# Optimization experiments

Measured on AMD Instinct MI355X. Metric: run time of the kernel, lower is better.

## Reference

```python
import jax, jax.numpy as jnp
import numpy as np

B, M, N, P, H, W, D, DIMG, NH = 32, 2048, 512, 16, 640, 640, 256, 384, 8
PD = 3 * P * P  # 768 flattened patch dim


def layer_norm(x, g, b, eps=1e-5):
    mu = x.mean(-1, keepdims=True)
    var = ((x - mu) ** 2).mean(-1, keepdims=True)
    return (x - mu) * jax.lax.rsqrt(var + eps) * g + b


def get_patches(img, kpts, patch):
    # img [B,3,H,W], kpts [B,N,2] (x,y), NaN rows -> NaN patches
    Bb, C, Hh, Ww = img.shape
    half = patch // 2
    safe = jnp.nan_to_num(kpts, nan=0.0)
    ctr = jnp.round(safe).astype(jnp.int32)
    x0 = jnp.clip(ctr[..., 0] - half, 0, Ww - patch)
    y0 = jnp.clip(ctr[..., 1] - half, 0, Hh - patch)
    offs = jnp.arange(patch)
    ys = y0[..., None] + offs  # [B,N,P]
    xs = x0[..., None] + offs  # [B,N,P]

    def ext(im_b, ys_b, xs_b):
        p = im_b[:, ys_b[:, :, None], xs_b[:, None, :]]  # [C,N,P,P]
        return jnp.transpose(p, (1, 0, 2, 3))  # [N,C,P,P]

    patches = jax.vmap(ext)(img, ys, xs)  # [B,N,C,P,P]
    invalid = jnp.isnan(kpts).any(-1)
    return jnp.where(invalid[:, :, None, None, None], jnp.nan, patches)


def setup_inputs() -> dict:
    key = jax.random.key(0)
    ks = jax.random.split(key, 16)
    im0 = jax.random.uniform(ks[0], (B, 3, H, W), jnp.float32)
    im1 = jax.random.uniform(ks[1], (B, 3, H, W), jnp.float32)
    wh = jnp.array([W - 1.0, H - 1.0], jnp.float32)
    kpts0 = jax.random.uniform(ks[2], (B, M, 2), jnp.float32) * wh
    kpts1 = jax.random.uniform(ks[3], (B, M, 2), jnp.float32) * wh
    scores0 = jax.random.uniform(ks[4], (B, M), jnp.float32)
    scores1 = jax.random.uniform(ks[5], (B, M), jnp.float32)
    image_embs = jax.random.normal(ks[6], (B, DIMG), jnp.float32)
    m0 = jax.random.randint(ks[7], (B, N), 0, M)
    m1 = jax.random.randint(ks[8], (B, N), -300, M)
    m1 = jnp.where(m1 < 0, -1, m1)
    sorted_matches = jnp.stack([m0, m1], axis=-1).astype(jnp.int32)
    s = 0.02
    params = dict(
        ln1_g=jnp.ones((PD,), jnp.float32), ln1_b=jnp.zeros((PD,), jnp.float32),
        W_pe=jax.random.normal(ks[9], (D - 1, PD), jnp.float32) * s,
        b_pe=jnp.zeros((D - 1,), jnp.float32),
        ln2_g=jnp.ones((D - 1,), jnp.float32), ln2_b=jnp.zeros((D - 1,), jnp.float32),
        W_proj=jax.random.normal(ks[10], (D, DIMG), jnp.float32) * s,
        b_proj=jnp.zeros((D,), jnp.float32),
        in_w=jax.random.normal(ks[11], (3 * D, D), jnp.float32) * s,
        in_b=jnp.zeros((3 * D,), jnp.float32),
        out_w=jax.random.normal(ks[12], (D, D), jnp.float32) * s,
        out_b=jnp.zeros((D,), jnp.float32),
        W_fc=jax.random.normal(ks[13], (6, D), jnp.float32) * s,
        b_fc=jnp.zeros((6,), jnp.float32),
    )
    return dict(im0=im0, im1=im1, kpts0=kpts0, kpts1=kpts1, scores0=scores0,
                scores1=scores1, image_embs=image_embs,
                sorted_matches=sorted_matches, **params)


def reference(im0, im1, kpts0, kpts1, scores0, scores1, image_embs,
              sorted_matches, ln1_g, ln1_b, W_pe, b_pe, ln2_g, ln2_b,
              W_proj, b_proj, in_w, in_b, out_w, out_b, W_fc, b_fc):
    im0 = jnp.clip(im0, 0.0, 1.0)
    im1 = jnp.clip(im1, 0.0, 1.0)
    m0 = sorted_matches[..., 0]
    m1 = sorted_matches[..., 1]
    valid = m1 > -1  # [B,N]
    m0c = jnp.clip(m0, 0, M - 1)
    m1c = jnp.clip(m1, 0, M - 1)
    # vectorized masked gather with NaN padding (replaces the double python loop)
    g0 = jnp.take_along_axis(kpts0, m0c[..., None], axis=1)  # [B,N,2]
    g1 = jnp.take_along_axis(kpts1, m1c[..., None], axis=1)
    k0v = jnp.where(valid[..., None], g0, jnp.nan)
    k1v = jnp.where(valid[..., None], g1, jnp.nan)
    s0v = jnp.where(valid, jnp.take_along_axis(scores0, m0c, axis=1), 0.0)
    s1v = jnp.where(valid, jnp.take_along_axis(scores1, m1c, axis=1), 0.0)
    p0 = jnp.nan_to_num(get_patches(im0, k0v, P), nan=-1.0)  # [B,N,3,P,P]
    p1 = jnp.nan_to_num(get_patches(im1, k1v, P), nan=-1.0)
    patches = jnp.concatenate([p0, p1], axis=1)  # [B,2N,3,P,P]
    flat = patches.reshape(B, 2 * N, PD)
    e = layer_norm(flat, ln1_g, ln1_b)
    e = e @ W_pe.T + b_pe
    e = layer_norm(e, ln2_g, ln2_b)  # [B,2N,D-1]
    scores = jnp.concatenate([s0v, s1v], axis=1)  # [B,2N]
    pe = jnp.concatenate([e, scores[..., None]], axis=-1)  # [B,2N,D]
    # motion estimator: cross-attn, query = projected image embedding
    q = image_embs @ W_proj.T + b_proj  # [B,D]
    Wq, Wk, Wv = in_w[:D], in_w[D:2 * D], in_w[2 * D:]
    bq, bk, bv = in_b[:D], in_b[D:2 * D], in_b[2 * D:]
    dh = D // NH
    qh = (q @ Wq.T + bq).reshape(B, 1, NH, dh)
    kh = (pe @ Wk.T + bk).reshape(B, 2 * N, NH, dh)
    vh = (pe @ Wv.T + bv).reshape(B, 2 * N, NH, dh)
    scale = 1.0 / np.sqrt(dh).astype(np.float32)
    att = jnp.einsum('bqhd,bkhd->bhqk', qh, kh) * scale
    a = jax.nn.softmax(att, axis=-1)
    o = jnp.einsum('bhqk,bkhd->bqhd', a, vh).reshape(B, 1, D)
    o = o @ out_w.T + out_b
    out = (o @ W_fc.T + b_fc).reshape(B, 6)
    return out
```

## Files before the change

kernel.cpp:

```cpp
#include <hip/hip_runtime.h>
#include <math.h>

#define BB 32
#define MM 2048
#define NN 512
#define PSZ 16
#define HH 640
#define WW 640
#define DD 256
#define DIMG_ 384
#define NHEADS 8
#define PD_ 768
#define TWO_N 1024
#define ROWS_TOT (BB * TWO_N)
#define CHCT 16

typedef short bf16x8 __attribute__((ext_vector_type(8)));
typedef float f32x4  __attribute__((ext_vector_type(4)));

__device__ __forceinline__ unsigned short f2bf(float x) {
  unsigned int u = __float_as_uint(x);
  u = (u + 0x7FFF + ((u >> 16) & 1)) >> 16;
  return (unsigned short)u;
}
__device__ __forceinline__ float bf2f(unsigned short h) {
  return __uint_as_float(((unsigned int)h) << 16);
}

__device__ __forceinline__ void gload_lds16(const void* g, void* l) {
  __builtin_amdgcn_global_load_lds(
      (const __attribute__((address_space(1))) void*)g,
      (__attribute__((address_space(3))) void*)l, 16, 0, 0);
}

__global__ __launch_bounds__(256) void prep_extract_kernel(
    const float* __restrict__ W_pe,
    unsigned short* __restrict__ Whi, unsigned short* __restrict__ Wlo,
    const float* __restrict__ image_embs,
    const float* __restrict__ W_proj, const float* __restrict__ b_proj,
    const float* __restrict__ in_w,   const float* __restrict__ in_b,
    float* __restrict__ u_out, float* __restrict__ bias_out,
    const float* __restrict__ im0, const float* __restrict__ im1,
    const float* __restrict__ kpts0, const float* __restrict__ kpts1,
    const float* __restrict__ scores0, const float* __restrict__ scores1,
    const int*   __restrict__ sorted_matches,
    const float* __restrict__ ln1_g, const float* __restrict__ ln1_b,
    unsigned short* __restrict__ Ahi, unsigned short* __restrict__ Alo,
    float* __restrict__ score_all)
{
  __shared__ float q1[DD];
  __shared__ float q2[DD];
  const int t = threadIdx.x;

  if (blockIdx.x < 768) {
    const int idx = blockIdx.x * 256 + t;
    const int row = idx / PD_;
    float v = (row < 255) ? W_pe[idx] : 0.0f;
    const unsigned short h = f2bf(v);
    Whi[idx] = h;
    Wlo[idx] = f2bf(v - bf2f(h));
    return;
  }

  if (blockIdx.x < 800) {
    const int b = blockIdx.x - 768;
    {
      const float4* emb = (const float4*)(image_embs + (size_t)b * DIMG_);
      const float4* wr  = (const float4*)(W_proj + (size_t)t * DIMG_);
      float a = b_proj[t];
      #pragma unroll 4
      for (int i = 0; i < DIMG_ / 4; ++i) {
        const float4 e4 = emb[i], w4 = wr[i];
        a += e4.x * w4.x + e4.y * w4.y + e4.z * w4.z + e4.w * w4.w;
      }
      q1[t] = a;
    }
    __syncthreads();
    {
      const float4* wr = (const float4*)(in_w + (size_t)t * DD);
      const float4* qq = (const float4*)q1;
      float a = in_b[t];
      #pragma unroll 4
      for (int i = 0; i < DD / 4; ++i) {
        const float4 q4 = qq[i], w4 = wr[i];
        a += q4.x * w4.x + q4.y * w4.y + q4.z * w4.z + q4.w * w4.w;
      }
      q2[t] = a;
    }
    __syncthreads();
    #pragma unroll
    for (int h = 0; h < NHEADS; ++h) {
      float s = 0.0f;
      #pragma unroll 8
      for (int i = 0; i < 32; ++i)
        s += q2[h * 32 + i] * in_w[(size_t)(DD + h * 32 + i) * DD + t];
      u_out[((size_t)b * NHEADS + h) * DD + t] = s;
    }
    if (t < NHEADS) {
      float s = 0.0f;
      for (int i = 0; i < 32; ++i) s += q2[t * 32 + i] * in_b[DD + t * 32 + i];
      bias_out[b * NHEADS + t] = s;
    }
    return;
  }

  const int L  = t & 63;
  const long gp = (long)(blockIdx.x - 800) * 4 + (t >> 6);
  const int b   = (int)(gp >> 10);
  const int n2  = (int)(gp & 1023);
  const bool side1 = (n2 >= NN);
  const float* img  = side1 ? im1 : im0;
  const float* kpts = side1 ? kpts1 : kpts0;
  const float* scrs = side1 ? scores1 : scores0;

  const int n  = side1 ? (n2 - NN) : n2;
  const int m0 = sorted_matches[((size_t)b * NN + n) * 2 + 0];
  const int m1 = sorted_matches[((size_t)b * NN + n) * 2 + 1];
  const bool valid = (m1 > -1);
  int midx = side1 ? m1 : m0;
  midx = min(max(midx, 0), MM - 1);
  const float kx = kpts[((size_t)b * MM + midx) * 2 + 0];
  const float ky = kpts[((size_t)b * MM + midx) * 2 + 1];
  const int x0 = min(max((int)rintf(kx) - 8, 0), WW - PSZ);
  const int y0 = min(max((int)rintf(ky) - 8, 0), HH - PSZ);

  float v[12];
  if (valid) {
    const size_t imb = (size_t)b * 3 * HH * WW;
    const int px = (2 * L) & 15;
    #pragma unroll
    for (int j = 0; j < 6; ++j) {
      const int p0 = 2 * L + 128 * j;
      const int c  = p0 >> 8;
      const int py = (p0 >> 4) & 15;
      const float* rp = img + imb + ((size_t)c * HH + y0 + py) * WW + x0 + px;
      v[2 * j]     = fminf(fmaxf(rp[0], 0.0f), 1.0f);
      v[2 * j + 1] = fminf(fmaxf(rp[1], 0.0f), 1.0f);
    }
  } else {
    #pragma unroll
    for (int i = 0; i < 12; ++i) v[i] = -1.0f;
  }

  float s = 0.0f, ss = 0.0f;
  #pragma unroll
  for (int i = 0; i < 12; ++i) { s += v[i]; ss += v[i] * v[i]; }
  #pragma unroll
  for (int m = 32; m; m >>= 1) { s += __shfl_xor(s, m); ss += __shfl_xor(ss, m); }
  const float mu  = s * (1.0f / 768.0f);
  const float var = ss * (1.0f / 768.0f) - mu * mu;
  const float rs  = 1.0f / sqrtf(var + 1e-5f);

  unsigned int* AhiW = (unsigned int*)(Ahi + gp * PD_);
  unsigned int* AloW = (unsigned int*)(Alo + gp * PD_);
  #pragma unroll
  for (int j = 0; j < 6; ++j) {
    const int p0 = 2 * L + 128 * j;
    const float y0e = (v[2 * j]     - mu) * rs * ln1_g[p0]     + ln1_b[p0];
    const float y1e = (v[2 * j + 1] - mu) * rs * ln1_g[p0 + 1] + ln1_b[p0 + 1];
    const unsigned short h0 = f2bf(y0e), h1 = f2bf(y1e);
    AhiW[p0 >> 1] = (unsigned int)h0 | ((unsigned int)h1 << 16);
    const unsigned short l0 = f2bf(y0e - bf2f(h0));
    const unsigned short l1 = f2bf(y1e - bf2f(h1));
    AloW[p0 >> 1] = (unsigned int)l0 | ((unsigned int)l1 << 16);
  }
  if (L == 0) {
    score_all[gp] = valid ? scrs[(size_t)b * MM + midx] : 0.0f;
  }
}

__global__ __launch_bounds__(512, 1) void gemm_fused_kernel(
    const unsigned short* __restrict__ Ahi, const unsigned short* __restrict__ Alo,
    const unsigned short* __restrict__ Whi, const unsigned short* __restrict__ Wlo,
    const float* __restrict__ b_pe,
    const float* __restrict__ ln2_g, const float* __restrict__ ln2_b,
    const float* __restrict__ score_all,
    const float* __restrict__ u, const float* __restrict__ ubias,
    float* __restrict__ pe, float* __restrict__ lt)
{
  __shared__ __align__(16) char smem[98304];
  __shared__ float u_lds[NHEADS * DD];
  __shared__ float cv_bpe[DD], cv_g[DD], cv_b[DD];
  __shared__ float ub_lds[NHEADS];

  unsigned short* const sbase = (unsigned short*)smem;
  const int t = threadIdx.x;
  const int w = t >> 6, L = t & 63;
  const int mt = blockIdx.x;
  const int bidx = mt >> 3;

  {
    const float* ub0 = u + (size_t)bidx * NHEADS * DD;
    #pragma unroll
    for (int i = 0; i < 4; ++i) u_lds[t + 512 * i] = ub0[t + 512 * i];
    if (t < DD) {
      cv_bpe[t] = (t < 255) ? b_pe[t]  : 0.0f;
      cv_g[t]   = (t < 255) ? ln2_g[t] : 0.0f;
      cv_b[t]   = (t < 255) ? ln2_b[t] : 0.0f;
    }
    if (t < NHEADS) ub_lds[t] = ubias[bidx * NHEADS + t];
  }

  const int rr   = L >> 2;
  const int q_st = (L & 3) ^ ((L >> 4) & 3);

  const unsigned short* gsrc[6];
  int loff0[6], sstr[6];
  #pragma unroll
  for (int c = 0; c < 6; ++c) {
    const int cc = w * 6 + c;
    const unsigned short* sp; long row; int off, str;
    if (cc < 16) {
      sp  = (cc < 8) ? Ahi : Alo;
      row = (long)mt * 128 + (cc & 7) * 16 + rr;
      off = ((cc >> 3) * 128 + (cc & 7) * 16) * 32;
      str = 8192;
    } else {
      const int c2 = cc - 16;
      sp  = (c2 < 16) ? Whi : Wlo;
      row = (c2 & 15) * 16 + rr;
      off = 16384 + ((c2 >> 4) * 256 + (c2 & 15) * 16) * 32;
      str = 16384;
    }
    gsrc[c]  = sp + row * (long)PD_ + q_st * 8;
    loff0[c] = off;
    sstr[c]  = str;
  }

  const int lane_m = L & 15, quad = L >> 4;
  const int swz = quad ^ (lane_m >> 2);
  const int wr = w >> 2, wc = w & 3;
  const int am0 = wr * 64, bn0 = wc * 64;

  f32x4 acc[4][4];
  #pragma unroll
  for (int i = 0; i < 4; ++i)
    #pragma unroll
    for (int j = 0; j < 4; ++j) acc[i][j] = (f32x4){0.f, 0.f, 0.f, 0.f};

  #pragma unroll
  for (int c = 0; c < 6; ++c) gload_lds16(gsrc[c], sbase + loff0[c]);
  __syncthreads();

  for (int ks = 0; ks < PD_ / 32; ++ks) {
    const int cur = ks & 1;
    if (ks < PD_ / 32 - 1) {
      const int k0n = (ks + 1) * 32;
      const int nb  = cur ^ 1;
      #pragma unroll
      for (int c = 0; c < 6; ++c)
        gload_lds16(gsrc[c] + k0n, sbase + loff0[c] + nb * sstr[c]);
    }
    const unsigned short* Ab = sbase + cur * 8192;
    const unsigned short* Bb = sbase + 16384 + cur * 16384;
    bf16x8 ah[4], al[4], bh[4], bl[4];
    #pragma unroll
    for (int i = 0; i < 4; ++i) {
      const int ra = (am0 + i * 16 + lane_m) * 32 + swz * 8;
      ah[i] = *(const bf16x8*)(Ab + ra);
      al[i] = *(const bf16x8*)(Ab + 4096 + ra);
      const int rb = (bn0 + i * 16 + lane_m) * 32 + swz * 8;
      bh[i] = *(const bf16x8*)(Bb + rb);
      bl[i] = *(const bf16x8*)(Bb + 8192 + rb);
    }
    #pragma unroll
    for (int i = 0; i < 4; ++i)
      #pragma unroll
      for (int j = 0; j < 4; ++j) {
        acc[i][j] = __builtin_amdgcn_mfma_f32_16x16x32_bf16(ah[i], bh[j], acc[i][j], 0, 0, 0);
        acc[i][j] = __builtin_amdgcn_mfma_f32_16x16x32_bf16(ah[i], bl[j], acc[i][j], 0, 0, 0);
        acc[i][j] = __builtin_amdgcn_mfma_f32_16x16x32_bf16(al[i], bh[j], acc[i][j], 0, 0, 0);
      }
    __syncthreads();
  }

  float* const eb = (float*)smem;
  const int r8 = t >> 3, l8 = t & 7;
  #pragma unroll
  for (int hh = 0; hh < 2; ++hh) {
    if (hh) __syncthreads();
    if (wr == hh) {
      #pragma unroll
      for (int i = 0; i < 4; ++i)
        #pragma unroll
        for (int j = 0; j < 4; ++j)
          #pragma unroll
          for (int v = 0; v < 4; ++v)
            eb[(i * 16 + quad * 4 + v) * 260 + bn0 + j * 16 + lane_m] = acc[i][j][v];
    }
    __syncthreads();

    const long grow = (long)mt * 128 + hh * 64 + r8;
    float x[32];
    float s = 0.0f, ss = 0.0f;
    #pragma unroll
    for (int j = 0; j < 32; ++j) {
      const int c = l8 + 8 * j;
      float vv = eb[r8 * 260 + c];
      if (c < 255) { vv += cv_bpe[c]; s += vv; ss += vv * vv; }
      x[j] = vv;
    }
    s += __shfl_xor(s, 1); ss += __shfl_xor(ss, 1);
    s += __shfl_xor(s, 2); ss += __shfl_xor(ss, 2);
    s += __shfl_xor(s, 4); ss += __shfl_xor(ss, 4);
    const float mu  = s * (1.0f / 255.0f);
    const float var = ss * (1.0f / 255.0f) - mu * mu;
    const float rs  = 1.0f / sqrtf(var + 1e-5f);

    float scrow = 0.0f;
    if (l8 == 7) scrow = score_all[grow];

    float d[NHEADS] = {0, 0, 0, 0, 0, 0, 0, 0};
    float* const per = pe + grow * DD;
    #pragma unroll
    for (int j = 0; j < 32; ++j) {
      const int c = l8 + 8 * j;
      const float y = (c < 255) ? (x[j] - mu) * rs * cv_g[c] + cv_b[c] : scrow;
      per[c] = y;
      #pragma unroll
      for (int h = 0; h < NHEADS; ++h) d[h] += y * u_lds[h * DD + c];
    }
    #pragma unroll
    for (int h = 0; h < NHEADS; ++h) {
      d[h] += __shfl_xor(d[h], 1);
      d[h] += __shfl_xor(d[h], 2);
      d[h] += __shfl_xor(d[h], 4);
    }
    const float dv = (l8 == 0) ? d[0] : (l8 == 1) ? d[1] : (l8 == 2) ? d[2] :
                     (l8 == 3) ? d[3] : (l8 == 4) ? d[4] : (l8 == 5) ? d[5] :
                     (l8 == 6) ? d[6] : d[7];
    lt[grow * NHEADS + l8] = (dv + ub_lds[l8]) * 0.17677669529663687f;
  }
}

__global__ __launch_bounds__(256) void ctx_kernel(
    const float* __restrict__ pe, const float* __restrict__ lt,
    float* __restrict__ ctxp)
{
  __shared__ __align__(16) float pr[TWO_N][NHEADS];
  const int b = blockIdx.x, ch = blockIdx.y, t = threadIdx.x;

  {
    const int h = t >> 5, l = t & 31;
    const float* base = lt + (size_t)b * TWO_N * NHEADS + h;
    float v[32];
    float mx = -1e30f;
    #pragma unroll 8
    for (int i = 0; i < 32; ++i) { v[i] = base[(l + 32 * i) * NHEADS]; mx = fmaxf(mx, v[i]); }
    #pragma unroll
    for (int m = 16; m; m >>= 1) mx = fmaxf(mx, __shfl_xor(mx, m, 32));
    float sm = 0.0f;
    #pragma unroll 8
    for (int i = 0; i < 32; ++i) { v[i] = expf(v[i] - mx); sm += v[i]; }
    #pragma unroll
    for (int m = 16; m; m >>= 1) sm += __shfl_xor(sm, m, 32);
    const float inv = 1.0f / sm;
    #pragma unroll 8
    for (int i = 0; i < 32; ++i) pr[l + 32 * i][h] = v[i] * inv;
  }
  __syncthreads();

  const float* peb = pe + ((size_t)b * TWO_N + ch * 64) * DD;
  float acc[NHEADS] = {0, 0, 0, 0, 0, 0, 0, 0};
  #pragma unroll 4
  for (int k = 0; k < 64; ++k) {
    const float v = peb[(size_t)k * DD + t];
    const float4 a0 = *(const float4*)&pr[ch * 64 + k][0];
    const float4 a1 = *(const float4*)&pr[ch * 64 + k][4];
    acc[0] += a0.x * v; acc[1] += a0.y * v; acc[2] += a0.z * v; acc[3] += a0.w * v;
    acc[4] += a1.x * v; acc[5] += a1.y * v; acc[6] += a1.z * v; acc[7] += a1.w * v;
  }
  #pragma unroll
  for (int h = 0; h < NHEADS; ++h)
    ctxp[(((size_t)b * CHCT + ch) * NHEADS + h) * DD + t] = acc[h];
}

__global__ __launch_bounds__(256) void final_kernel(
    const float* __restrict__ ctxp,
    const float* __restrict__ in_w,  const float* __restrict__ in_b,
    const float* __restrict__ out_w, const float* __restrict__ out_b,
    const float* __restrict__ W_fc,  const float* __restrict__ b_fc,
    float* __restrict__ outp)
{
  __shared__ __align__(16) float ctx_sh[NHEADS * DD];
  __shared__ __align__(16) float o_sh[DD], o2_sh[DD];
  const int t = threadIdx.x;
  const int b = blockIdx.x;

  #pragma unroll
  for (int h = 0; h < NHEADS; ++h) {
    float s = 0.0f;
    #pragma unroll
    for (int ch = 0; ch < CHCT; ++ch)
      s += ctxp[(((size_t)b * CHCT + ch) * NHEADS + h) * DD + t];
    ctx_sh[h * DD + t] = s;
  }
  __syncthreads();
  {
    const float4* wv = (const float4*)(in_w + (size_t)(2 * DD + t) * DD);
    const float4* cx = (const float4*)(ctx_sh + (t >> 5) * DD);
    float o1 = in_b[2 * DD + t];
    #pragma unroll 4
    for (int j = 0; j < DD / 4; ++j) {
      const float4 w4 = wv[j], c4 = cx[j];
      o1 += w4.x * c4.x + w4.y * c4.y + w4.z * c4.z + w4.w * c4.w;
    }
    o_sh[t] = o1;
  }
  __syncthreads();
  {
    const float4* wr = (const float4*)(out_w + (size_t)t * DD);
    const float4* oo = (const float4*)o_sh;
    float o2 = out_b[t];
    #pragma unroll 4
    for (int j = 0; j < DD / 4; ++j) {
      const float4 w4 = wr[j], c4 = oo[j];
      o2 += w4.x * c4.x + w4.y * c4.y + w4.z * c4.z + w4.w * c4.w;
    }
    o2_sh[t] = o2;
  }
  __syncthreads();
  if (t < 6) {
    const float4* wr = (const float4*)(W_fc + (size_t)t * DD);
    const float4* oo = (const float4*)o2_sh;
    float r = b_fc[t];
    for (int j = 0; j < DD / 4; ++j) {
      const float4 w4 = wr[j], c4 = oo[j];
      r += w4.x * c4.x + w4.y * c4.y + w4.z * c4.z + w4.w * c4.w;
    }
    outp[b * 6 + t] = r;
  }
}

extern "C" void kernel_launch(void* const* d_in, const int* in_sizes, int n_in,
                              void* d_out, int out_size, void* d_ws, size_t ws_size,
                              hipStream_t stream) {
  const float* im0       = (const float*)d_in[0];
  const float* im1       = (const float*)d_in[1];
  const float* kpts0     = (const float*)d_in[2];
  const float* kpts1     = (const float*)d_in[3];
  const float* scores0   = (const float*)d_in[4];
  const float* scores1   = (const float*)d_in[5];
  const float* image_embs= (const float*)d_in[6];
  const int*   smatch    = (const int*)d_in[7];
  const float* ln1_g     = (const float*)d_in[8];
  const float* ln1_b     = (const float*)d_in[9];
  const float* W_pe      = (const float*)d_in[10];
  const float* b_pe      = (const float*)d_in[11];
  const float* ln2_g     = (const float*)d_in[12];
  const float* ln2_b     = (const float*)d_in[13];
  const float* W_proj    = (const float*)d_in[14];
  const float* b_proj    = (const float*)d_in[15];
  const float* in_w      = (const float*)d_in[16];
  const float* in_b      = (const float*)d_in[17];
  const float* out_w     = (const float*)d_in[18];
  const float* out_b     = (const float*)d_in[19];
  const float* W_fc      = (const float*)d_in[20];
  const float* b_fc      = (const float*)d_in[21];

  char* ws = (char*)d_ws;
  size_t off = 0;
  float* epe   = (float*)(ws + off); off += (size_t)ROWS_TOT * DD * 4;
  float* u     = (float*)(ws + off); off += (size_t)BB * NHEADS * DD * 4;
  float* ubias = (float*)(ws + off); off += (size_t)BB * NHEADS * 4;
  off = (off + 1023) & ~(size_t)1023;
  float* score = (float*)(ws + off); off += (size_t)ROWS_TOT * 4;
  float* lt    = (float*)(ws + off); off += (size_t)BB * TWO_N * NHEADS * 4;
  float* ctxp  = (float*)(ws + off); off += (size_t)BB * CHCT * NHEADS * DD * 4;
  unsigned short* Whi = (unsigned short*)(ws + off); off += (size_t)256 * PD_ * 2;
  unsigned short* Wlo = (unsigned short*)(ws + off); off += (size_t)256 * PD_ * 2;
  off = (off + 1023) & ~(size_t)1023;
  unsigned short* Ahi = (unsigned short*)(ws + off); off += (size_t)ROWS_TOT * PD_ * 2;
  unsigned short* Alo = (unsigned short*)(ws + off); off += (size_t)ROWS_TOT * PD_ * 2;

  prep_extract_kernel<<<800 + ROWS_TOT / 4, 256, 0, stream>>>(
      W_pe, Whi, Wlo, image_embs, W_proj, b_proj, in_w, in_b, u, ubias,
      im0, im1, kpts0, kpts1, scores0, scores1, smatch,
      ln1_g, ln1_b, Ahi, Alo, score);
  gemm_fused_kernel<<<ROWS_TOT / 128, 512, 0, stream>>>(
      Ahi, Alo, Whi, Wlo, b_pe, ln2_g, ln2_b, score, u, ubias, epe, lt);
  ctx_kernel<<<dim3(BB, CHCT), 256, 0, stream>>>(epe, lt, ctxp);
  final_kernel<<<BB, 256, 0, stream>>>(ctxp, in_w, in_b, out_w, out_b,
                                       W_fc, b_fc, (float*)d_out);
}
```

Before: 510.0 us.

## Fold attention-logit projection into GEMM via precomputed per-batch V columns

The per-head logit dot product with u is rewritten algebraically. Per-batch vectors V = W_pe^T (g*u) are precomputed in the prep kernel and appended as 16 extra B columns, so the GEMM produces the logit term directly and the LayerNorm correction is applied with precomputed scalar sums. This removes the per-row 8-head dot product over 255 columns in the epilogue. The GEMM is also retiled to 64-row blocks with 256 threads, two blocks per CU, a single LDS buffer and no double buffering. Softmax moves into its own kernel so ctx uses more, smaller chunks. Precision shifts slightly because the logits now depend on split-bf16 products of V.

```diff
diff --git a/kernel.cpp b/kernel.cpp
--- a/kernel.cpp
+++ b/kernel.cpp
@@ -13,7 +13,7 @@
 #define PD_ 768
 #define TWO_N 1024
 #define ROWS_TOT (BB * TWO_N)
-#define CHCT 16
+#define CHCT 32
 
 typedef short bf16x8 __attribute__((ext_vector_type(8)));
 typedef float f32x4  __attribute__((ext_vector_type(4)));
@@ -39,7 +39,10 @@
     const float* __restrict__ image_embs,
     const float* __restrict__ W_proj, const float* __restrict__ b_proj,
     const float* __restrict__ in_w,   const float* __restrict__ in_b,
-    float* __restrict__ u_out, float* __restrict__ bias_out,
+    const float* __restrict__ b_pe,
+    const float* __restrict__ ln2_g, const float* __restrict__ ln2_b,
+    unsigned short* __restrict__ Vhi, unsigned short* __restrict__ Vlo,
+    float* __restrict__ Pc,
     const float* __restrict__ im0, const float* __restrict__ im1,
     const float* __restrict__ kpts0, const float* __restrict__ kpts1,
     const float* __restrict__ scores0, const float* __restrict__ scores1,
@@ -49,7 +52,10 @@
     float* __restrict__ score_all)
 {
   __shared__ float q1[DD];
-  __shared__ float q2[DD];
+  __shared__ float q2s[DD];
+  __shared__ float u_sh[NHEADS][DD];
+  __shared__ float gu_sh[DD][NHEADS];
+  __shared__ float sred[NHEADS][3][4];
   const int t = threadIdx.x;
 
   if (blockIdx.x < 768) {
@@ -85,7 +91,7 @@
         const float4 q4 = qq[i], w4 = wr[i];
         a += q4.x * w4.x + q4.y * w4.y + q4.z * w4.z + q4.w * w4.w;
       }
-      q2[t] = a;
+      q2s[t] = a;
     }
     __syncthreads();
     #pragma unroll
@@ -93,13 +99,67 @@
       float s = 0.0f;
       #pragma unroll 8
       for (int i = 0; i < 32; ++i)
-        s += q2[h * 32 + i] * in_w[(size_t)(DD + h * 32 + i) * DD + t];
-      u_out[((size_t)b * NHEADS + h) * DD + t] = s;
-    }
+        s += q2s[h * 32 + i] * in_w[(size_t)(DD + h * 32 + i) * DD + t];
+      u_sh[h][t] = s;
+    }
+    float ubv = 0.0f;
     if (t < NHEADS) {
-      float s = 0.0f;
-      for (int i = 0; i < 32; ++i) s += q2[t * 32 + i] * in_b[DD + t * 32 + i];
-      bias_out[b * NHEADS + t] = s;
+      for (int i = 0; i < 32; ++i) ubv += q2s[t * 32 + i] * in_b[DD + t * 32 + i];
+    }
+    __syncthreads();
+
+    const bool cvld = (t < 255);
+    const float g_c = cvld ? ln2_g[t] : 0.0f;
+    const float bb_c = cvld ? ln2_b[t] : 0.0f;
+    const float pp_c = cvld ? b_pe[t]  : 0.0f;
+    const int wv = t >> 6, ln = t & 63;
+    #pragma unroll
+    for (int h = 0; h < NHEADS; ++h) {
+      const float u_c = u_sh[h][t];
+      const float gu  = g_c * u_c;
+      gu_sh[t][h] = gu;
+      float x1 = gu, x2 = bb_c * u_c, x3 = pp_c * gu;
+      #pragma unroll
+      for (int m = 32; m; m >>= 1) {
+        x1 += __shfl_xor(x1, m); x2 += __shfl_xor(x2, m); x3 += __shfl_xor(x3, m);
+      }
+      if (ln == 0) { sred[h][0][wv] = x1; sred[h][1][wv] = x2; sred[h][2][wv] = x3; }
+    }
+    __syncthreads();
+    if (t < NHEADS) {
+      const float S1 = sred[t][0][0] + sred[t][0][1] + sred[t][0][2] + sred[t][0][3];
+      const float S2 = sred[t][1][0] + sred[t][1][1] + sred[t][1][2] + sred[t][1][3];
+      const float S3 = sred[t][2][0] + sred[t][2][1] + sred[t][2][2] + sred[t][2][3];
+      float* pc = Pc + b * 40;
+      pc[t]      = S1;
+      pc[8 + t]  = S2;
+      pc[16 + t] = S3;
+      pc[24 + t] = u_sh[t][255];
+      pc[32 + t] = ubv;
+    }
+
+    #pragma unroll
+    for (int kk = 0; kk < 3; ++kk) {
+      const int k = t + 256 * kk;
+      float vh[NHEADS] = {0, 0, 0, 0, 0, 0, 0, 0};
+      for (int c = 0; c < 255; ++c) {
+        const float wv_ = W_pe[(size_t)c * PD_ + k];
+        const float4 g0 = *(const float4*)&gu_sh[c][0];
+        const float4 g1 = *(const float4*)&gu_sh[c][4];
+        vh[0] += wv_ * g0.x; vh[1] += wv_ * g0.y; vh[2] += wv_ * g0.z; vh[3] += wv_ * g0.w;
+        vh[4] += wv_ * g1.x; vh[5] += wv_ * g1.y; vh[6] += wv_ * g1.z; vh[7] += wv_ * g1.w;
+      }
+      #pragma unroll
+      for (int h = 0; h < NHEADS; ++h) {
+        const unsigned short hi = f2bf(vh[h]);
+        Vhi[((size_t)b * 16 + h) * PD_ + k] = hi;
+        Vlo[((size_t)b * 16 + h) * PD_ + k] = f2bf(vh[h] - bf2f(hi));
+      }
+      #pragma unroll
+      for (int h = NHEADS; h < 16; ++h) {
+        Vhi[((size_t)b * 16 + h) * PD_ + k] = 0;
+        Vlo[((size_t)b * 16 + h) * PD_ + k] = 0;
+      }
     }
     return;
   }
@@ -169,204 +229,212 @@
   }
 }
 
-__global__ __launch_bounds__(512, 1) void gemm_fused_kernel(
+__global__ __launch_bounds__(256, 2) void gemm_fused_kernel(
     const unsigned short* __restrict__ Ahi, const unsigned short* __restrict__ Alo,
     const unsigned short* __restrict__ Whi, const unsigned short* __restrict__ Wlo,
+    const unsigned short* __restrict__ Vhi, const unsigned short* __restrict__ Vlo,
     const float* __restrict__ b_pe,
     const float* __restrict__ ln2_g, const float* __restrict__ ln2_b,
     const float* __restrict__ score_all,
-    const float* __restrict__ u, const float* __restrict__ ubias,
+    const float* __restrict__ Pc,
     float* __restrict__ pe, float* __restrict__ lt)
 {
-  __shared__ __align__(16) char smem[98304];
-  __shared__ float u_lds[NHEADS * DD];
-  __shared__ float cv_bpe[DD], cv_g[DD], cv_b[DD];
-  __shared__ float ub_lds[NHEADS];
-
-  unsigned short* const sbase = (unsigned short*)smem;
+  __shared__ __align__(16) unsigned short sm[21504];
   const int t = threadIdx.x;
   const int w = t >> 6, L = t & 63;
   const int mt = blockIdx.x;
-  const int bidx = mt >> 3;
-
-  {
-    const float* ub0 = u + (size_t)bidx * NHEADS * DD;
-    #pragma unroll
-    for (int i = 0; i < 4; ++i) u_lds[t + 512 * i] = ub0[t + 512 * i];
-    if (t < DD) {
-      cv_bpe[t] = (t < 255) ? b_pe[t]  : 0.0f;
-      cv_g[t]   = (t < 255) ? ln2_g[t] : 0.0f;
-      cv_b[t]   = (t < 255) ? ln2_b[t] : 0.0f;
-    }
-    if (t < NHEADS) ub_lds[t] = ubias[bidx * NHEADS + t];
-  }
+  const int bidx = mt >> 4;
 
   const int rr   = L >> 2;
   const int q_st = (L & 3) ^ ((L >> 4) & 3);
-
-  const unsigned short* gsrc[6];
-  int loff0[6], sstr[6];
-  #pragma unroll
-  for (int c = 0; c < 6; ++c) {
-    const int cc = w * 6 + c;
-    const unsigned short* sp; long row; int off, str;
-    if (cc < 16) {
-      sp  = (cc < 8) ? Ahi : Alo;
-      row = (long)mt * 128 + (cc & 7) * 16 + rr;
-      off = ((cc >> 3) * 128 + (cc & 7) * 16) * 32;
-      str = 8192;
-    } else {
-      const int c2 = cc - 16;
-      sp  = (c2 < 16) ? Whi : Wlo;
-      row = (c2 & 15) * 16 + rr;
-      off = 16384 + ((c2 >> 4) * 256 + (c2 & 15) * 16) * 32;
-      str = 16384;
-    }
-    gsrc[c]  = sp + row * (long)PD_ + q_st * 8;
-    loff0[c] = off;
-    sstr[c]  = str;
-  }
-
   const int lane_m = L & 15, quad = L >> 4;
   const int swz = quad ^ (lane_m >> 2);
-  const int wr = w >> 2, wc = w & 3;
-  const int am0 = wr * 64, bn0 = wc * 64;
-
-  f32x4 acc[4][4];
+
+  const unsigned short* gsrc[11];
+  int ldst[11];
+  #pragma unroll
+  for (int c = 0; c < 11; ++c) {
+    const int cc = w + 4 * c;
+    const unsigned short* sp = Ahi; long rb = 0; int dst = 0;
+    if (cc < 4)       { sp = Ahi; rb = (long)mt * 64 + cc * 16;       dst = cc * 512; }
+    else if (cc < 8)  { sp = Alo; rb = (long)mt * 64 + (cc - 4) * 16; dst = 2048 + (cc - 4) * 512; }
+    else if (cc < 25) { const int r0 = (cc - 8) * 16;
+                        sp = (r0 < 256) ? (Whi + (long)r0 * PD_)
+                                        : (Vhi + (long)bidx * 16 * PD_);
+                        dst = 4096 + (cc - 8) * 512; }
+    else if (cc < 42) { const int r0 = (cc - 25) * 16;
+                        sp = (r0 < 256) ? (Wlo + (long)r0 * PD_)
+                                        : (Vlo + (long)bidx * 16 * PD_);
+                        dst = 12800 + (cc - 25) * 512; }
+    gsrc[c] = sp + (rb + rr) * (long)PD_ + q_st * 8;
+    ldst[c] = dst;
+  }
+  const int CNT = (w < 2) ? 11 : 10;
+  const int JW  = (w == 3) ? 5 : 4;
+
+  f32x4 acc[4][5];
   #pragma unroll
   for (int i = 0; i < 4; ++i)
     #pragma unroll
-    for (int j = 0; j < 4; ++j) acc[i][j] = (f32x4){0.f, 0.f, 0.f, 0.f};
-
-  #pragma unroll
-  for (int c = 0; c < 6; ++c) gload_lds16(gsrc[c], sbase + loff0[c]);
-  __syncthreads();
+    for (int j = 0; j < 5; ++j) acc[i][j] = (f32x4){0.f, 0.f, 0.f, 0.f};
 
   for (int ks = 0; ks < PD_ / 32; ++ks) {
-    const int cur = ks & 1;
-    if (ks < PD_ / 32 - 1) {
-      const int k0n = (ks + 1) * 32;
-      const int nb  = cur ^ 1;
+    const int k0 = ks * 32;
+    __syncthreads();
+    #pragma unroll
+    for (int c = 0; c < 11; ++c)
+      if (c < CNT) gload_lds16(gsrc[c] + k0, sm + ldst[c]);
+    __syncthreads();
+
+    bf16x8 ah[4], al[4];
+    #pragma unroll
+    for (int i = 0; i < 4; ++i) {
+      const int offa = (i * 16 + lane_m) * 32 + swz * 8;
+      ah[i] = *(const bf16x8*)(sm + offa);
+      al[i] = *(const bf16x8*)(sm + 2048 + offa);
+    }
+    #pragma unroll
+    for (int j = 0; j < 5; ++j) {
+      if (j < JW) {
+        const int offb = (w * 64 + j * 16 + lane_m) * 32 + swz * 8;
+        const bf16x8 bh = *(const bf16x8*)(sm + 4096 + offb);
+        const bf16x8 bl = *(const bf16x8*)(sm + 12800 + offb);
+        #pragma unroll
+        for (int i = 0; i < 4; ++i) {
+          acc[i][j] = __builtin_amdgcn_mfma_f32_16x16x32_bf16(ah[i], bh, acc[i][j], 0, 0, 0);
+          acc[i][j] = __builtin_amdgcn_mfma_f32_16x16x32_bf16(ah[i], bl, acc[i][j], 0, 0, 0);
+          acc[i][j] = __builtin_amdgcn_mfma_f32_16x16x32_bf16(al[i], bh, acc[i][j], 0, 0, 0);
+        }
+      }
+    }
+  }
+
+  __syncthreads();
+  float* const fs = (float*)sm;
+  float p4[4], g4[4], b4[4];
+  #pragma unroll
+  for (int j = 0; j < 4; ++j) {
+    const int c = w * 64 + j * 16 + lane_m;
+    const bool cv = (c < 255);
+    p4[j] = cv ? b_pe[c]  : 0.0f;
+    g4[j] = cv ? ln2_g[c] : 0.0f;
+    b4[j] = cv ? ln2_b[c] : 0.0f;
+  }
+  float sv[16], qv[16];
+  #pragma unroll
+  for (int i = 0; i < 4; ++i)
+    #pragma unroll
+    for (int v = 0; v < 4; ++v) {
+      float s = 0.0f, q = 0.0f;
       #pragma unroll
-      for (int c = 0; c < 6; ++c)
-        gload_lds16(gsrc[c] + k0n, sbase + loff0[c] + nb * sstr[c]);
-    }
-    const unsigned short* Ab = sbase + cur * 8192;
-    const unsigned short* Bb = sbase + 16384 + cur * 16384;
-    bf16x8 ah[4], al[4], bh[4], bl[4];
-    #pragma unroll
-    for (int i = 0; i < 4; ++i) {
-      const int ra = (am0 + i * 16 + lane_m) * 32 + swz * 8;
-      ah[i] = *(const bf16x8*)(Ab + ra);
-      al[i] = *(const bf16x8*)(Ab + 4096 + ra);
-      const int rb = (bn0 + i * 16 + lane_m) * 32 + swz * 8;
-      bh[i] = *(const bf16x8*)(Bb + rb);
-      bl[i] = *(const bf16x8*)(Bb + 8192 + rb);
-    }
+      for (int j = 0; j < 4; ++j) {
+        const float x = acc[i][j][v] + p4[j];
+        s += x; q += x * x;
+      }
+      sv[i * 4 + v] = s; qv[i * 4 + v] = q;
+    }
+  #pragma unroll
+  for (int iv = 0; iv < 16; ++iv) {
+    #pragma unroll
+    for (int m = 1; m <= 8; m <<= 1) {
+      sv[iv] += __shfl_xor(sv[iv], m);
+      qv[iv] += __shfl_xor(qv[iv], m);
+    }
+  }
+  if (lane_m == 0) {
     #pragma unroll
     for (int i = 0; i < 4; ++i)
       #pragma unroll
+      for (int v = 0; v < 4; ++v) {
+        const int row = i * 16 + quad * 4 + v;
+        fs[w * 64 + row]       = sv[i * 4 + v];
+        fs[256 + w * 64 + row] = qv[i * 4 + v];
+      }
+  }
+  __syncthreads();
+  if (t < 64) {
+    const float S  = fs[t] + fs[64 + t] + fs[128 + t] + fs[192 + t];
+    const float SS = fs[256 + t] + fs[320 + t] + fs[384 + t] + fs[448 + t];
+    const float mu  = S * (1.0f / 255.0f);
+    const float var = SS * (1.0f / 255.0f) - mu * mu;
+    fs[512 + t] = mu;
+    fs[576 + t] = 1.0f / sqrtf(var + 1e-5f);
+  }
+  __syncthreads();
+
+  float S1 = 0, S2 = 0, S3 = 0, u255 = 0, ubias = 0;
+  if (w == 3 && lane_m < NHEADS) {
+    const float* pc = Pc + bidx * 40;
+    S1 = pc[lane_m]; S2 = pc[8 + lane_m]; S3 = pc[16 + lane_m];
+    u255 = pc[24 + lane_m]; ubias = pc[32 + lane_m];
+  }
+
+  #pragma unroll
+  for (int i = 0; i < 4; ++i)
+    #pragma unroll
+    for (int v = 0; v < 4; ++v) {
+      const int row = i * 16 + quad * 4 + v;
+      const long grow = (long)mt * 64 + row;
+      const float mu = fs[512 + row];
+      const float rs = fs[576 + row];
+      float sc = 0.0f;
+      if (w == 3) sc = score_all[grow];
+      float* rowp = pe + grow * DD + w * 64 + lane_m;
+      #pragma unroll
       for (int j = 0; j < 4; ++j) {
-        acc[i][j] = __builtin_amdgcn_mfma_f32_16x16x32_bf16(ah[i], bh[j], acc[i][j], 0, 0, 0);
-        acc[i][j] = __builtin_amdgcn_mfma_f32_16x16x32_bf16(ah[i], bl[j], acc[i][j], 0, 0, 0);
-        acc[i][j] = __builtin_amdgcn_mfma_f32_16x16x32_bf16(al[i], bh[j], acc[i][j], 0, 0, 0);
-      }
-    __syncthreads();
-  }
-
-  float* const eb = (float*)smem;
-  const int r8 = t >> 3, l8 = t & 7;
-  #pragma unroll
-  for (int hh = 0; hh < 2; ++hh) {
-    if (hh) __syncthreads();
-    if (wr == hh) {
-      #pragma unroll
-      for (int i = 0; i < 4; ++i)
-        #pragma unroll
-        for (int j = 0; j < 4; ++j)
-          #pragma unroll
-          for (int v = 0; v < 4; ++v)
-            eb[(i * 16 + quad * 4 + v) * 260 + bn0 + j * 16 + lane_m] = acc[i][j][v];
-    }
-    __syncthreads();
-
-    const long grow = (long)mt * 128 + hh * 64 + r8;
-    float x[32];
-    float s = 0.0f, ss = 0.0f;
-    #pragma unroll
-    for (int j = 0; j < 32; ++j) {
-      const int c = l8 + 8 * j;
-      float vv = eb[r8 * 260 + c];
-      if (c < 255) { vv += cv_bpe[c]; s += vv; ss += vv * vv; }
-      x[j] = vv;
-    }
-    s += __shfl_xor(s, 1); ss += __shfl_xor(ss, 1);
-    s += __shfl_xor(s, 2); ss += __shfl_xor(ss, 2);
-    s += __shfl_xor(s, 4); ss += __shfl_xor(ss, 4);
-    const float mu  = s * (1.0f / 255.0f);
-    const float var = ss * (1.0f / 255.0f) - mu * mu;
-    const float rs  = 1.0f / sqrtf(var + 1e-5f);
-
-    float scrow = 0.0f;
-    if (l8 == 7) scrow = score_all[grow];
-
-    float d[NHEADS] = {0, 0, 0, 0, 0, 0, 0, 0};
-    float* const per = pe + grow * DD;
-    #pragma unroll
-    for (int j = 0; j < 32; ++j) {
-      const int c = l8 + 8 * j;
-      const float y = (c < 255) ? (x[j] - mu) * rs * cv_g[c] + cv_b[c] : scrow;
-      per[c] = y;
-      #pragma unroll
-      for (int h = 0; h < NHEADS; ++h) d[h] += y * u_lds[h * DD + c];
-    }
-    #pragma unroll
-    for (int h = 0; h < NHEADS; ++h) {
-      d[h] += __shfl_xor(d[h], 1);
-      d[h] += __shfl_xor(d[h], 2);
-      d[h] += __shfl_xor(d[h], 4);
-    }
-    const float dv = (l8 == 0) ? d[0] : (l8 == 1) ? d[1] : (l8 == 2) ? d[2] :
-                     (l8 == 3) ? d[3] : (l8 == 4) ? d[4] : (l8 == 5) ? d[5] :
-                     (l8 == 6) ? d[6] : d[7];
-    lt[grow * NHEADS + l8] = (dv + ub_lds[l8]) * 0.17677669529663687f;
-  }
+        const int c = w * 64 + j * 16 + lane_m;
+        const float y = (c < 255)
+            ? (acc[i][j][v] + p4[j] - mu) * rs * g4[j] + b4[j]
+            : sc;
+        rowp[j * 16] = y;
+      }
+      if (w == 3 && lane_m < NHEADS) {
+        const float T = acc[i][4][v];
+        const float d = rs * (T + S3 - mu * S1) + S2 + sc * u255;
+        lt[grow * NHEADS + lane_m] = (d + ubias) * 0.17677669529663687f;
+      }
+    }
+}
+
+__global__ __launch_bounds__(256) void softmax_kernel(
+    const float* __restrict__ lt, float* __restrict__ prg)
+{
+  const int b = blockIdx.x, t = threadIdx.x;
+  const int h = t >> 5, l = t & 31;
+  const float* base = lt + (size_t)b * TWO_N * NHEADS + h;
+  float v[32];
+  float mx = -1e30f;
+  #pragma unroll 8
+  for (int i = 0; i < 32; ++i) { v[i] = base[(l + 32 * i) * NHEADS]; mx = fmaxf(mx, v[i]); }
+  #pragma unroll
+  for (int m = 16; m; m >>= 1) mx = fmaxf(mx, __shfl_xor(mx, m, 32));
+  float sm = 0.0f;
+  #pragma unroll 8
+  for (int i = 0; i < 32; ++i) { v[i] = expf(v[i] - mx); sm += v[i]; }
+  #pragma unroll
+  for (int m = 16; m; m >>= 1) sm += __shfl_xor(sm, m, 32);
+  const float inv = 1.0f / sm;
+  float* out = prg + (size_t)b * TWO_N * NHEADS + h;
+  #pragma unroll 8
+  for (int i = 0; i < 32; ++i) out[(l + 32 * i) * NHEADS] = v[i] * inv;
 }
 
 __global__ __launch_bounds__(256) void ctx_kernel(
-    const float* __restrict__ pe, const float* __restrict__ lt,
+    const float* __restrict__ pe, const float* __restrict__ prg,
     float* __restrict__ ctxp)
 {
-  __shared__ __align__(16) float pr[TWO_N][NHEADS];
+  __shared__ __align__(16) float prc[32 * NHEADS];
   const int b = blockIdx.x, ch = blockIdx.y, t = threadIdx.x;
-
-  {
-    const int h = t >> 5, l = t & 31;
-    const float* base = lt + (size_t)b * TWO_N * NHEADS + h;
-    float v[32];
-    float mx = -1e30f;
-    #pragma unroll 8
-    for (int i = 0; i < 32; ++i) { v[i] = base[(l + 32 * i) * NHEADS]; mx = fmaxf(mx, v[i]); }
-    #pragma unroll
-    for (int m = 16; m; m >>= 1) mx = fmaxf(mx, __shfl_xor(mx, m, 32));
-    float sm = 0.0f;
-    #pragma unroll 8
-    for (int i = 0; i < 32; ++i) { v[i] = expf(v[i] - mx); sm += v[i]; }
-    #pragma unroll
-    for (int m = 16; m; m >>= 1) sm += __shfl_xor(sm, m, 32);
-    const float inv = 1.0f / sm;
-    #pragma unroll 8
-    for (int i = 0; i < 32; ++i) pr[l + 32 * i][h] = v[i] * inv;
-  }
-  __syncthreads();
-
-  const float* peb = pe + ((size_t)b * TWO_N + ch * 64) * DD;
+  prc[t] = prg[((size_t)b * TWO_N + ch * 32) * NHEADS + t];
+  __syncthreads();
+
+  const float* peb = pe + ((size_t)b * TWO_N + ch * 32) * DD;
   float acc[NHEADS] = {0, 0, 0, 0, 0, 0, 0, 0};
   #pragma unroll 4
-  for (int k = 0; k < 64; ++k) {
+  for (int k = 0; k < 32; ++k) {
     const float v = peb[(size_t)k * DD + t];
-    const float4 a0 = *(const float4*)&pr[ch * 64 + k][0];
-    const float4 a1 = *(const float4*)&pr[ch * 64 + k][4];
+    const float4 a0 = *(const float4*)&prc[k * NHEADS];
+    const float4 a1 = *(const float4*)&prc[k * NHEADS + 4];
     acc[0] += a0.x * v; acc[1] += a0.y * v; acc[2] += a0.z * v; acc[3] += a0.w * v;
     acc[4] += a1.x * v; acc[5] += a1.y * v; acc[6] += a1.z * v; acc[7] += a1.w * v;
   }
@@ -461,25 +529,29 @@
   char* ws = (char*)d_ws;
   size_t off = 0;
   float* epe   = (float*)(ws + off); off += (size_t)ROWS_TOT * DD * 4;
-  float* u     = (float*)(ws + off); off += (size_t)BB * NHEADS * DD * 4;
-  float* ubias = (float*)(ws + off); off += (size_t)BB * NHEADS * 4;
-  off = (off + 1023) & ~(size_t)1023;
   float* score = (float*)(ws + off); off += (size_t)ROWS_TOT * 4;
   float* lt    = (float*)(ws + off); off += (size_t)BB * TWO_N * NHEADS * 4;
+  float* prg   = (float*)(ws + off); off += (size_t)BB * TWO_N * NHEADS * 4;
   float* ctxp  = (float*)(ws + off); off += (size_t)BB * CHCT * NHEADS * DD * 4;
+  float* Pc    = (float*)(ws + off); off += (size_t)BB * 40 * 4;
+  off = (off + 1023) & ~(size_t)1023;
   unsigned short* Whi = (unsigned short*)(ws + off); off += (size_t)256 * PD_ * 2;
   unsigned short* Wlo = (unsigned short*)(ws + off); off += (size_t)256 * PD_ * 2;
+  unsigned short* Vhi = (unsigned short*)(ws + off); off += (size_t)BB * 16 * PD_ * 2;
+  unsigned short* Vlo = (unsigned short*)(ws + off); off += (size_t)BB * 16 * PD_ * 2;
   off = (off + 1023) & ~(size_t)1023;
   unsigned short* Ahi = (unsigned short*)(ws + off); off += (size_t)ROWS_TOT * PD_ * 2;
   unsigned short* Alo = (unsigned short*)(ws + off); off += (size_t)ROWS_TOT * PD_ * 2;
 
   prep_extract_kernel<<<800 + ROWS_TOT / 4, 256, 0, stream>>>(
-      W_pe, Whi, Wlo, image_embs, W_proj, b_proj, in_w, in_b, u, ubias,
+      W_pe, Whi, Wlo, image_embs, W_proj, b_proj, in_w, in_b,
+      b_pe, ln2_g, ln2_b, Vhi, Vlo, Pc,
       im0, im1, kpts0, kpts1, scores0, scores1, smatch,
       ln1_g, ln1_b, Ahi, Alo, score);
-  gemm_fused_kernel<<<ROWS_TOT / 128, 512, 0, stream>>>(
-      Ahi, Alo, Whi, Wlo, b_pe, ln2_g, ln2_b, score, u, ubias, epe, lt);
-  ctx_kernel<<<dim3(BB, CHCT), 256, 0, stream>>>(epe, lt, ctxp);
+  gemm_fused_kernel<<<ROWS_TOT / 64, 256, 0, stream>>>(
+      Ahi, Alo, Whi, Wlo, Vhi, Vlo, b_pe, ln2_g, ln2_b, score, Pc, epe, lt);
+  softmax_kernel<<<BB, 256, 0, stream>>>(lt, prg);
+  ctx_kernel<<<dim3(BB, CHCT), 256, 0, stream>>>(epe, prg, ctxp);
   final_kernel<<<BB, 256, 0, stream>>>(ctxp, in_w, in_b, out_w, out_b,
                                        W_fc, b_fc, (float*)d_out);
 }
```

New measurement: 545.0 us. 6.9% more time.
